# Performance work log

Hardware: AMD Instinct MI355X
Metric: run time of the kernel (lower is better)

## Reference

```python
import jax, jax.numpy as jnp
import numpy as np

B, L, D, H = 2, 2048, 2048, 16
Dh = D // H
THETA = 10000.0
NEG = -1e9


def _rope_tables(length, offset=0):
    # inv_freq: [Dh/2], positions: [L]
    inv_freq = 1.0 / (THETA ** (jnp.arange(0, Dh, 2, dtype=jnp.float32) / Dh))
    pos = jnp.arange(offset, offset + length, dtype=jnp.float32)
    freqs = pos[:, None] * inv_freq[None, :]           # [L, Dh/2]
    emb = jnp.concatenate([freqs, freqs], axis=-1)     # [L, Dh]
    return jnp.cos(emb), jnp.sin(emb)


def _rotate_half(t):
    t1, t2 = t[..., : Dh // 2], t[..., Dh // 2:]
    return jnp.concatenate([-t2, t1], axis=-1)


def setup_inputs() -> dict:
    key = jax.random.key(0)
    k1, k2, k3 = jax.random.split(key, 3)
    x = jax.random.normal(k1, (B, L, D), dtype=jnp.float32)
    attention_mask = jnp.ones((B, L), dtype=jnp.int32)
    w_qkv = jax.random.normal(k2, (D, 3 * D), dtype=jnp.float32) * (D ** -0.5)
    w_proj = jax.random.normal(k3, (D, D), dtype=jnp.float32) * (D ** -0.5)
    return {"x": x, "attention_mask": attention_mask, "w_qkv": w_qkv, "w_proj": w_proj}


def reference(x, attention_mask, w_qkv, w_proj):
    # QKV projection (no bias)
    qkv = x @ w_qkv                                    # [B, L, 3D]
    q, k, v = jnp.split(qkv, 3, axis=-1)
    q = q.reshape(B, L, H, Dh).transpose(0, 2, 1, 3)   # [B, H, L, Dh]
    k = k.reshape(B, L, H, Dh).transpose(0, 2, 1, 3)
    v = v.reshape(B, L, H, Dh).transpose(0, 2, 1, 3)

    # RoPE (past_len = 0)
    cos, sin = _rope_tables(L)                         # [L, Dh]
    q = q * cos + _rotate_half(q) * sin
    k = k * cos + _rotate_half(k) * sin

    # causal + key-padding mask (True = masked out)
    causal = jnp.triu(jnp.ones((L, L), dtype=bool), k=1)         # [L, L]
    pad = (attention_mask == 0)[:, None, None, :]                # [B,1,1,L]
    mask = causal[None, None, :, :] | pad                        # [B,1,L,L]

    scale = Dh ** -0.5
    scores = jnp.einsum("bhqd,bhkd->bhqk", q, k) * scale         # [B,H,L,L]
    scores = jnp.where(mask, NEG, scores)
    attn = jax.nn.softmax(scores, axis=-1)
    y = jnp.einsum("bhqk,bhkd->bhqd", attn, v)                   # [B,H,L,Dh]
    y = y.transpose(0, 2, 1, 3).reshape(B, L, D)
    return y @ w_proj
```

## Files before the change

kernel.cpp:

```cpp
#include <hip/hip_runtime.h>
#include <hip/hip_bf16.h>

typedef unsigned short ushort_t;
typedef __attribute__((ext_vector_type(4))) float fvec4;
typedef __attribute__((ext_vector_type(16))) float fvec16;
typedef __attribute__((ext_vector_type(8))) short short8;
typedef __attribute__((ext_vector_type(4))) unsigned short usvec4;
typedef __attribute__((ext_vector_type(2))) unsigned int uvec2;

typedef const __attribute__((address_space(1))) void* gas_ptr;
typedef __attribute__((address_space(3))) void* las_ptr;

__device__ __forceinline__ void glds16(const void* g, void* l) {
  __builtin_amdgcn_global_load_lds((gas_ptr)g, (las_ptr)l, 16, 0, 0);
}

__device__ __forceinline__ ushort_t f2bf(float f) {
  unsigned u = __float_as_uint(f);
  u += 0x7FFFu + ((u >> 16) & 1u);
  return (ushort_t)(u >> 16);
}
__device__ __forceinline__ float bf2f(ushort_t h) {
  return __uint_as_float(((unsigned)h) << 16);
}

__device__ __forceinline__ void swap32(unsigned& a, unsigned& b) {
#if __has_builtin(__builtin_amdgcn_permlane32_swap)
  uvec2 r = __builtin_amdgcn_permlane32_swap(a, b, false, false);
  a = r[0]; b = r[1];
#else
  const unsigned sa = (unsigned)__shfl_xor((int)a, 32);
  const unsigned sb = (unsigned)__shfl_xor((int)b, 32);
  const bool hi = (threadIdx.x & 32) != 0;
  const unsigned na = hi ? sb : a;
  const unsigned nb = hi ? b : sa;
  a = na; b = nb;
#endif
}

__global__ __launch_bounds__(256) void cast_f32_bf16(const float* __restrict__ X,
                                                     ushort_t* __restrict__ Xb) {
  const size_t i = ((size_t)blockIdx.x * 256 + threadIdx.x) * 4;
  const fvec4 v = *(const fvec4*)(X + i);
  usvec4 o;
  o[0] = f2bf(v[0]); o[1] = f2bf(v[1]); o[2] = f2bf(v[2]); o[3] = f2bf(v[3]);
  *(usvec4*)(Xb + i) = o;
}

__global__ __launch_bounds__(256) void tcast(const float* __restrict__ W,
                                             ushort_t* __restrict__ Wt,
                                             const int Kd, const int Nd) {
  __shared__ float ls[64][65];
  const int t = threadIdx.x;
  const int n0 = blockIdx.x * 64, k0 = blockIdx.y * 64;
  const int kr = t >> 4, nc = (t & 15) * 4;
#pragma unroll
  for (int it = 0; it < 4; ++it) {
    const fvec4 v = *(const fvec4*)(W + (size_t)(k0 + it * 16 + kr) * Nd + n0 + nc);
    ls[it * 16 + kr][nc + 0] = v[0];
    ls[it * 16 + kr][nc + 1] = v[1];
    ls[it * 16 + kr][nc + 2] = v[2];
    ls[it * 16 + kr][nc + 3] = v[3];
  }
  __syncthreads();
  const int nr = t >> 2, kg = (t & 3) * 16;
  __align__(16) ushort_t tmp[16];
#pragma unroll
  for (int i = 0; i < 16; ++i) tmp[i] = f2bf(ls[kg + i][nr]);
  ushort_t* dst = Wt + (size_t)(n0 + nr) * Kd + k0 + kg;
  *(short8*)(dst)     = *(const short8*)(tmp);
  *(short8*)(dst + 8) = *(const short8*)(tmp + 8);
}

__device__ __forceinline__ void stage_unit(const ushort_t* __restrict__ G, const int rbase,
                                           const int K, const int tk,
                                           ushort_t* ldsmat, const int u,
                                           const int wv, const int lane) {
  const int rr = lane >> 3;
  const int kk = ((lane & 7) ^ rr) * 8;
  const int r64 = wv * 8 + rr;
  glds16(G + (size_t)(rbase + u * 64 + r64) * K + tk + kk,
         ldsmat + (((u * 2 + 0) * 64 + wv * 8) * 64));
  glds16(G + (size_t)(rbase + 128 + u * 64 + r64) * K + tk + kk,
         ldsmat + (((u * 2 + 1) * 64 + wv * 8) * 64));
}

__device__ __forceinline__ short8 frag_ld(const ushort_t* ldsmat, const int rbase,
                                          const int kc, const int quad, const int mm) {
  const int r = rbase + mm;
  const int blk = r >> 6;
  const int pblk = ((blk & 1) << 1) | (blk >> 1);
  const int ldsrow = pblk * 64 + (r & 63);
  const int kb = (kc * 64 + quad * 16) ^ ((mm & 7) << 4);
  return *(const short8*)(ldsmat + ldsrow * 64 + (kb >> 1));
}

#define FENCE asm volatile("" ::: "memory")

#define LD_A4(s_, q_)                                                         \
  short8 af[2][2];                                                            \
  af[0][0] = frag_ld(&lds[s_][0][0], wr * 128 + (q_) * 32,      0, quad, mm); \
  af[0][1] = frag_ld(&lds[s_][0][0], wr * 128 + (q_) * 32,      1, quad, mm); \
  af[1][0] = frag_ld(&lds[s_][0][0], wr * 128 + (q_) * 32 + 16, 0, quad, mm); \
  af[1][1] = frag_ld(&lds[s_][0][0], wr * 128 + (q_) * 32 + 16, 1, quad, mm);

#define LD_B8(s_)                                                             \
  _Pragma("unroll")                                                           \
  for (int j = 0; j < 4; ++j) {                                               \
    bfr[j][0] = frag_ld(&lds[s_][1][0], wc * 64 + j * 16, 0, quad, mm);       \
    bfr[j][1] = frag_ld(&lds[s_][1][0], wc * 64 + j * 16, 1, quad, mm);       \
  }

#define MFMA16(q_)                                                            \
  __builtin_amdgcn_s_setprio(1);                                              \
  _Pragma("unroll")                                                           \
  for (int ii = 0; ii < 2; ++ii)                                              \
  _Pragma("unroll")                                                           \
  for (int j = 0; j < 4; ++j) {                                               \
    acc[(q_) * 2 + ii][j] = __builtin_amdgcn_mfma_f32_16x16x32_bf16(          \
        af[ii][0], bfr[j][0], acc[(q_) * 2 + ii][j], 0, 0, 0);                \
    acc[(q_) * 2 + ii][j] = __builtin_amdgcn_mfma_f32_16x16x32_bf16(          \
        af[ii][1], bfr[j][1], acc[(q_) * 2 + ii][j], 0, 0, 0);                \
  }                                                                           \
  __builtin_amdgcn_s_setprio(0);

__global__ __launch_bounds__(512, 2) void gemm256(
    const ushort_t* __restrict__ A, const ushort_t* __restrict__ Bt,
    const int M, const int N, const int K, const int mode,
    float* __restrict__ C,
    ushort_t* __restrict__ Qo, ushort_t* __restrict__ Ko, ushort_t* __restrict__ Vo) {
  __shared__ __align__(16) ushort_t lds[2][2][16384];

  const int tid = threadIdx.x, wv = tid >> 6, lane = tid & 63;
  const int quad = lane >> 4, mm = lane & 15;
  const int wr = wv >> 2, wc = wv & 3;

  const int nwg = gridDim.x, ntx = N >> 8;
  const int bid = blockIdx.x;
  const int swz = (bid & 7) * (nwg >> 3) + (bid >> 3);
  const int by = swz / ntx, bx = swz - by * ntx;
  const int row0 = by * 256, col0 = bx * 256;

  fvec4 acc[8][4];
#pragma unroll
  for (int i = 0; i < 8; ++i)
#pragma unroll
    for (int j = 0; j < 4; ++j) acc[i][j] = (fvec4){0.f, 0.f, 0.f, 0.f};

  short8 bfr[4][2];

  stage_unit(Bt, col0, K, 0,  &lds[0][1][0], 0, wv, lane); FENCE;
  stage_unit(Bt, col0, K, 0,  &lds[0][1][0], 1, wv, lane); FENCE;
  stage_unit(A,  row0, K, 0,  &lds[0][0][0], 0, wv, lane); FENCE;
  stage_unit(A,  row0, K, 0,  &lds[0][0][0], 1, wv, lane); FENCE;
  stage_unit(Bt, col0, K, 64, &lds[1][1][0], 0, wv, lane); FENCE;
  stage_unit(Bt, col0, K, 64, &lds[1][1][0], 1, wv, lane); FENCE;
  stage_unit(A,  row0, K, 64, &lds[1][0][0], 0, wv, lane); FENCE;
  asm volatile("s_waitcnt vmcnt(6)" ::: "memory");
  __builtin_amdgcn_s_barrier();

  const int nit = K >> 7;
  for (int i = 0; i < nit; ++i) {
    const bool more = (i + 1 < nit);
    const int kA = i * 128 + 64;
    const int kB = i * 128 + 128;
    const int kC = i * 128 + 192;
    {
      __builtin_amdgcn_s_barrier();
      LD_A4(0, 0);
      LD_B8(0);
      stage_unit(A, row0, K, kA, &lds[1][0][0], 1, wv, lane);
      MFMA16(0);
    }
    {
      __builtin_amdgcn_s_barrier();
      LD_A4(0, 1);
      if (more) stage_unit(Bt, col0, K, kB, &lds[0][1][0], 0, wv, lane);
      MFMA16(1);
    }
    {
      __builtin_amdgcn_s_barrier();
      LD_A4(0, 2);
      if (more) stage_unit(Bt, col0, K, kB, &lds[0][1][0], 1, wv, lane);
      MFMA16(2);
    }
    {
      __builtin_amdgcn_s_barrier();
      LD_A4(0, 3);
      if (more) {
        stage_unit(A, row0, K, kB, &lds[0][0][0], 0, wv, lane);
        asm volatile("s_waitcnt vmcnt(6)" ::: "memory");
      } else {
        asm volatile("s_waitcnt vmcnt(0)" ::: "memory");
      }
      MFMA16(3);
    }
    {
      __builtin_amdgcn_s_barrier();
      LD_A4(1, 0);
      LD_B8(1);
      if (more) stage_unit(A, row0, K, kB, &lds[0][0][0], 1, wv, lane);
      MFMA16(0);
    }
    {
      __builtin_amdgcn_s_barrier();
      LD_A4(1, 1);
      if (more) stage_unit(Bt, col0, K, kC, &lds[1][1][0], 0, wv, lane);
      MFMA16(1);
    }
    {
      __builtin_amdgcn_s_barrier();
      LD_A4(1, 2);
      if (more) stage_unit(Bt, col0, K, kC, &lds[1][1][0], 1, wv, lane);
      MFMA16(2);
    }
    {
      __builtin_amdgcn_s_barrier();
      LD_A4(1, 3);
      if (more) {
        stage_unit(A, row0, K, kC, &lds[1][0][0], 0, wv, lane);
        asm volatile("s_waitcnt vmcnt(6)" ::: "memory");
      }
      MFMA16(3);
    }
  }

  if (mode == 0) {
#pragma unroll
    for (int i = 0; i < 8; ++i)
#pragma unroll
      for (int r = 0; r < 4; ++r) {
        const int row = row0 + wr * 128 + i * 16 + quad * 4 + r;
        float* cr = C + (size_t)row * N + col0 + wc * 64;
#pragma unroll
        for (int j = 0; j < 4; ++j) cr[j * 16 + mm] = acc[i][j][r];
      }
  } else {
    const int gcol = col0 + wc * 64;
    const int which = gcol >> 11;
    const int h = (gcol >> 7) & 15;
    const int coff = gcol & 127;
    ushort_t* dst = (which == 0) ? Qo : (which == 1) ? Ko : Vo;
#pragma unroll
    for (int i = 0; i < 8; ++i)
#pragma unroll
      for (int r = 0; r < 4; ++r) {
        const int row = row0 + wr * 128 + i * 16 + quad * 4 + r;
        const int bb = row >> 11, l = row & 2047;
        ushort_t* dr = dst + ((size_t)(bb * 16 + h) * 2048 + l) * 128 + coff;
#pragma unroll
        for (int j = 0; j < 4; ++j) dr[j * 16 + mm] = f2bf(acc[i][j][r]);
      }
  }
}

__global__ __launch_bounds__(256) void rope_kernel(ushort_t* Qb, ushort_t* Kb) {
  const int gid = blockIdx.x * 256 + threadIdx.x;
  const int pd = gid & 63;
  const int row = gid >> 6;
  const int l = row & 2047;
  ushort_t* base = (blockIdx.y ? Kb : Qb) + (size_t)row * 128;
  const float a = bf2f(base[pd]);
  const float bv = bf2f(base[pd + 64]);
  const float invf_rev = exp2f(-(float)pd * 0.20762050593045702f) * 0.15915494309189535f;
  float rev = (float)l * invf_rev;
  rev -= floorf(rev);
  const float ang = rev * 6.283185307179586f;
  float s, c;
  __sincosf(ang, &s, &c);
  float na = a * c - bv * s;
  float nb = bv * c + a * s;
  if (blockIdx.y == 0) { na *= 0.08838834764831845f; nb *= 0.08838834764831845f; }
  base[pd] = f2bf(na);
  base[pd + 64] = f2bf(nb);
}

__global__ __launch_bounds__(256) void vtrans_kernel(const ushort_t* __restrict__ Vn,
                                                     ushort_t* __restrict__ Vt) {
  __shared__ ushort_t ls[128 * 132];
  const int bh = blockIdx.x >> 4;
  const int l0 = (blockIdx.x & 15) * 128;
  const int t = threadIdx.x;
  const ushort_t* src = Vn + ((size_t)bh * 2048 + l0) * 128;
#pragma unroll
  for (int it = 0; it < 16; ++it) {
    const int c = it * 256 + t;
    const int lr = c >> 5, dc = (c & 31) * 4;
    *(usvec4*)(ls + lr * 132 + dc) = *(const usvec4*)(src + lr * 128 + dc);
  }
  __syncthreads();
  ushort_t* dstb = Vt + (size_t)bh * 128 * 2048 + l0;
#pragma unroll
  for (int it = 0; it < 16; ++it) {
    const int c = it * 256 + t;
    const int d = c >> 5, lc = (c & 31) * 4;
    usvec4 o;
    o[0] = ls[(lc + 0) * 132 + d];
    o[1] = ls[(lc + 1) * 132 + d];
    o[2] = ls[(lc + 2) * 132 + d];
    o[3] = ls[(lc + 3) * 132 + d];
    *(usvec4*)(dstb + (size_t)d * 2048 + lc) = o;
  }
}

__global__ __launch_bounds__(256, 2) void flash_kernel(
    const ushort_t* __restrict__ Qb, const ushort_t* __restrict__ Kb,
    const ushort_t* __restrict__ Vt, const int* __restrict__ am,
    ushort_t* __restrict__ Y) {
  __shared__ __align__(16) ushort_t lK[2][8192];
  __shared__ __align__(16) ushort_t lV[2][8192];
  __shared__ float lds_l[128];

  const int tid = threadIdx.x, wv = tid >> 6, lane = tid & 63;
  const int lh = lane >> 5, cq = lane & 31;
  const int bid = blockIdx.x;
  const int bh = bid & 31;
  const int qi = 15 - (bid >> 5);
  const int b = bh >> 4, head = bh & 15;
  const size_t qkBase = (size_t)bh * (2048 * 128);
  const int qb = qi * 128 + wv * 32;
  const int q = qb + cq;

  short8 qf[8];
  {
    const ushort_t* qrow = Qb + qkBase + (size_t)q * 128;
#pragma unroll
    for (int c = 0; c < 8; ++c) qf[c] = *(const short8*)(qrow + c * 16 + lh * 8);
  }

  fvec16 yacc[4];
#pragma unroll
  for (int i = 0; i < 4; ++i)
#pragma unroll
    for (int r = 0; r < 16; ++r) yacc[i][r] = 0.f;
  float psum = 0.f;

#define FLASH_STAGE(dK, dV, kk0)                                                          \
  _Pragma("unroll")                                                                       \
  for (int it = 0; it < 4; ++it) {                                                        \
    const int f_ = it * 4 + wv;                                                           \
    const int ct_ = f_ >> 3, c_ = f_ & 7;                                                 \
    glds16(Kb + qkBase + (size_t)((kk0) + ct_ * 32 + cq) * 128 + c_ * 16 + lh * 8,        \
           (dK) + f_ * 512);                                                              \
    const int dt_ = f_ >> 2, kc_ = f_ & 3;                                                \
    glds16(Vt + ((size_t)bh * 128 + dt_ * 32 + cq) * 2048 + (kk0) + kc_ * 16 + lh * 8,    \
           (dV) + f_ * 512);                                                              \
  }

  const int nt = qi * 2 + 2;
  FLASH_STAGE(&lK[0][0], &lV[0][0], 0)
  __syncthreads();

  int cur = 0;
  for (int t = 0; t < nt; ++t) {
    const int k0 = t * 64;
    if (t + 1 < nt) {
      FLASH_STAGE(&lK[cur ^ 1][0], &lV[cur ^ 1][0], k0 + 64)
    }

    if (k0 <= qb + 31) {
      const ushort_t* bK = &lK[cur][0];
      const ushort_t* bV = &lV[cur][0];
      const int amv = am[b * 2048 + k0 + lane];
      const unsigned long long keymask = __ballot(amv != 0);
      const bool fullvalid = (k0 + 63 <= qb) && (keymask == ~0ull);

#pragma unroll
      for (int ct = 0; ct < 2; ++ct) {
        fvec16 sacc;
#pragma unroll
        for (int r = 0; r < 16; ++r) sacc[r] = 0.f;
        __builtin_amdgcn_s_setprio(1);
#pragma unroll
        for (int c = 0; c < 8; ++c) {
          short8 kf = *(const short8*)(bK + (ct * 8 + c) * 512 + lane * 8);
          sacc = __builtin_amdgcn_mfma_f32_32x32x16_bf16(kf, qf[c], sacc, 0, 0, 0);
        }
        __builtin_amdgcn_s_setprio(0);
        float p[16];
        if (fullvalid) {
#pragma unroll
          for (int r = 0; r < 16; ++r) p[r] = __expf(sacc[r]);
        } else {
#pragma unroll
          for (int r = 0; r < 16; ++r) {
            const int kl = (r & 3) + 8 * (r >> 2) + 4 * lh + ct * 32;
            const bool ok = (k0 + kl <= q) && (((keymask >> kl) & 1ull) != 0);
            p[r] = ok ? __expf(sacc[r]) : 0.f;
          }
        }
#pragma unroll
        for (int r = 0; r < 16; ++r) psum += p[r];
        unsigned pk[8];
#pragma unroll
        for (int j = 0; j < 8; ++j) {
          __hip_bfloat162 t2 = __float22bfloat162_rn(make_float2(p[2 * j], p[2 * j + 1]));
          pk[j] = *(unsigned*)&t2;
        }
#pragma unroll
        for (int kc2 = 0; kc2 < 2; ++kc2) {
          unsigned a0 = pk[kc2 * 4 + 0], a2 = pk[kc2 * 4 + 2];
          unsigned a1 = pk[kc2 * 4 + 1], a3 = pk[kc2 * 4 + 3];
          swap32(a0, a2);
          swap32(a1, a3);
          union { unsigned u[4]; short8 s; } pf;
          pf.u[0] = a0; pf.u[1] = a1; pf.u[2] = a2; pf.u[3] = a3;
          const int kc = ct * 2 + kc2;
          __builtin_amdgcn_s_setprio(1);
#pragma unroll
          for (int dt = 0; dt < 4; ++dt) {
            short8 vf = *(const short8*)(bV + (dt * 4 + kc) * 512 + lane * 8);
            yacc[dt] = __builtin_amdgcn_mfma_f32_32x32x16_bf16(pf.s, vf, yacc[dt], 0, 0, 0);
          }
          __builtin_amdgcn_s_setprio(0);
        }
      }
    }
    __syncthreads();
    cur ^= 1;
  }
#undef FLASH_STAGE

  psum += __shfl_xor(psum, 32);
  if (lane < 32) lds_l[wv * 32 + lane] = psum;
  float inv16[16];
#pragma unroll
  for (int r = 0; r < 16; ++r)
    inv16[r] = 1.f / lds_l[wv * 32 + (r & 3) + 8 * (r >> 2) + 4 * lh];

#pragma unroll
  for (int dt = 0; dt < 4; ++dt)
#pragma unroll
    for (int r = 0; r < 16; ++r) {
      const int qloc = (r & 3) + 8 * (r >> 2) + 4 * lh;
      ushort_t* dst = Y + ((size_t)(b * 2048 + qb + qloc)) * 2048 + head * 128 + dt * 32 + cq;
      *dst = f2bf(yacc[dt][r] * inv16[r]);
    }
}

extern "C" void kernel_launch(void* const* d_in, const int* in_sizes, int n_in,
                              void* d_out, int out_size, void* d_ws, size_t ws_size,
                              hipStream_t stream) {
  const float* x      = (const float*)d_in[0];
  const int*   amask  = (const int*)d_in[1];
  const float* w_qkv  = (const float*)d_in[2];
  const float* w_proj = (const float*)d_in[3];

  ushort_t* xb     = (ushort_t*)d_ws;
  ushort_t* wqkvT  = xb + 8388608;
  ushort_t* wprojT = wqkvT + 12582912;
  ushort_t* Qb     = wprojT + 4194304;
  ushort_t* Kb     = Qb + 8388608;
  ushort_t* Vn     = Kb + 8388608;
  ushort_t* Vt     = wqkvT;
  ushort_t* Yb     = xb;

  cast_f32_bf16<<<8192, 256, 0, stream>>>(x, xb);
  tcast<<<dim3(96, 32), 256, 0, stream>>>(w_qkv, wqkvT, 2048, 6144);
  tcast<<<dim3(32, 32), 256, 0, stream>>>(w_proj, wprojT, 2048, 2048);
  gemm256<<<384, 512, 0, stream>>>(xb, wqkvT, 4096, 6144, 2048, 1,
                                   nullptr, Qb, Kb, Vn);
  rope_kernel<<<dim3(16384, 2), 256, 0, stream>>>(Qb, Kb);
  vtrans_kernel<<<512, 256, 0, stream>>>(Vn, Vt);
  flash_kernel<<<512, 256, 0, stream>>>(Qb, Kb, Vt, amask, Yb);
  gemm256<<<128, 512, 0, stream>>>(Yb, wprojT, 4096, 2048, 2048, 0,
                                   (float*)d_out, nullptr, nullptr, nullptr);
}
```

Measured before the change: 399.0 us.

## Add 128x256 GEMM kernel, precompute mask bits, split score MFMA chains

Adds a new gemm128 kernel with 128x256 tiles and two blocks per CU, and uses it for both the QKV and output projections. This doubles the grid to improve occupancy and wave balance across CUs, at the cost of less reuse per tile. In the flash kernel, per-tile attention-mask validity is precomputed once into a bitmask so each tile no longer issues a global load and ballot. The QK^T MFMA chain is also split into two independent accumulators to cut dependency latency, which adds one extra add per score.

```diff
diff --git a/kernel.cpp b/kernel.cpp
--- a/kernel.cpp
+++ b/kernel.cpp
@@ -72,6 +72,8 @@
   *(short8*)(dst + 8) = *(const short8*)(tmp + 8);
 }
 
+#define FENCE asm volatile("" ::: "memory")
+
 __device__ __forceinline__ void stage_unit(const ushort_t* __restrict__ G, const int rbase,
                                            const int K, const int tk,
                                            ushort_t* ldsmat, const int u,
@@ -94,8 +96,6 @@
   const int kb = (kc * 64 + quad * 16) ^ ((mm & 7) << 4);
   return *(const short8*)(ldsmat + ldsrow * 64 + (kb >> 1));
 }
-
-#define FENCE asm volatile("" ::: "memory")
 
 #define LD_A4(s_, q_)                                                         \
   short8 af[2][2];                                                            \
@@ -165,64 +165,41 @@
     const int kA = i * 128 + 64;
     const int kB = i * 128 + 128;
     const int kC = i * 128 + 192;
-    {
-      __builtin_amdgcn_s_barrier();
-      LD_A4(0, 0);
-      LD_B8(0);
+    { __builtin_amdgcn_s_barrier();
+      LD_A4(0, 0); LD_B8(0);
       stage_unit(A, row0, K, kA, &lds[1][0][0], 1, wv, lane);
-      MFMA16(0);
-    }
-    {
-      __builtin_amdgcn_s_barrier();
+      MFMA16(0); }
+    { __builtin_amdgcn_s_barrier();
       LD_A4(0, 1);
       if (more) stage_unit(Bt, col0, K, kB, &lds[0][1][0], 0, wv, lane);
-      MFMA16(1);
-    }
-    {
-      __builtin_amdgcn_s_barrier();
+      MFMA16(1); }
+    { __builtin_amdgcn_s_barrier();
       LD_A4(0, 2);
       if (more) stage_unit(Bt, col0, K, kB, &lds[0][1][0], 1, wv, lane);
-      MFMA16(2);
-    }
-    {
-      __builtin_amdgcn_s_barrier();
+      MFMA16(2); }
+    { __builtin_amdgcn_s_barrier();
       LD_A4(0, 3);
-      if (more) {
-        stage_unit(A, row0, K, kB, &lds[0][0][0], 0, wv, lane);
+      if (more) { stage_unit(A, row0, K, kB, &lds[0][0][0], 0, wv, lane);
         asm volatile("s_waitcnt vmcnt(6)" ::: "memory");
-      } else {
-        asm volatile("s_waitcnt vmcnt(0)" ::: "memory");
-      }
-      MFMA16(3);
-    }
-    {
-      __builtin_amdgcn_s_barrier();
-      LD_A4(1, 0);
-      LD_B8(1);
+      } else { asm volatile("s_waitcnt vmcnt(0)" ::: "memory"); }
+      MFMA16(3); }
+    { __builtin_amdgcn_s_barrier();
+      LD_A4(1, 0); LD_B8(1);
       if (more) stage_unit(A, row0, K, kB, &lds[0][0][0], 1, wv, lane);
-      MFMA16(0);
-    }
-    {
-      __builtin_amdgcn_s_barrier();
+      MFMA16(0); }
+    { __builtin_amdgcn_s_barrier();
       LD_A4(1, 1);
       if (more) stage_unit(Bt, col0, K, kC, &lds[1][1][0], 0, wv, lane);
-      MFMA16(1);
-    }
-    {
-      __builtin_amdgcn_s_barrier();
+      MFMA16(1); }
+    { __builtin_amdgcn_s_barrier();
       LD_A4(1, 2);
       if (more) stage_unit(Bt, col0, K, kC, &lds[1][1][0], 1, wv, lane);
-      MFMA16(2);
-    }
-    {
-      __builtin_amdgcn_s_barrier();
+      MFMA16(2); }
+    { __builtin_amdgcn_s_barrier();
       LD_A4(1, 3);
-      if (more) {
-        stage_unit(A, row0, K, kC, &lds[1][0][0], 0, wv, lane);
-        asm volatile("s_waitcnt vmcnt(6)" ::: "memory");
-      }
-      MFMA16(3);
-    }
+      if (more) { stage_unit(A, row0, K, kC, &lds[1][0][0], 0, wv, lane);
+        asm volatile("s_waitcnt vmcnt(6)" ::: "memory"); }
+      MFMA16(3); }
   }
 
   if (mode == 0) {
@@ -250,6 +227,178 @@
         ushort_t* dr = dst + ((size_t)(bb * 16 + h) * 2048 + l) * 128 + coff;
 #pragma unroll
         for (int j = 0; j < 4; ++j) dr[j * 16 + mm] = f2bf(acc[i][j][r]);
+      }
+  }
+}
+
+__device__ __forceinline__ void stage_a128(const ushort_t* __restrict__ G, const int row0,
+                                           const int K, const int tk, ushort_t* ldsA,
+                                           const int wv, const int lane) {
+  const int rr = lane >> 3;
+  const int kk = ((lane & 7) ^ rr) * 8;
+  const int r = wv * 8 + rr;
+  glds16(G + (size_t)(row0 + r) * K + tk + kk,      ldsA + (wv * 8) * 64);
+  glds16(G + (size_t)(row0 + 64 + r) * K + tk + kk, ldsA + (64 + wv * 8) * 64);
+}
+__device__ __forceinline__ void stage_b128(const ushort_t* __restrict__ G, const int col0,
+                                           const int K, const int tk, ushort_t* ldsB,
+                                           const int u, const int wv, const int lane) {
+  const int rr = lane >> 3;
+  const int kk = ((lane & 7) ^ rr) * 8;
+  const int r = u * 64 + wv * 8 + rr;
+  glds16(G + (size_t)(col0 + r) * K + tk + kk,       ldsB + (u * 64 + wv * 8) * 64);
+  glds16(G + (size_t)(col0 + 128 + r) * K + tk + kk, ldsB + (128 + u * 64 + wv * 8) * 64);
+}
+__device__ __forceinline__ short8 fragld128(const ushort_t* mat, const int row,
+                                            const int kc, const int quad) {
+  const int kb = (kc * 64 + quad * 16) ^ ((row & 7) << 4);
+  return *(const short8*)(mat + row * 64 + (kb >> 1));
+}
+
+__global__ __launch_bounds__(512, 2) void gemm128(
+    const ushort_t* __restrict__ A, const ushort_t* __restrict__ Bt,
+    const int M, const int N, const int K, const int mode,
+    float* __restrict__ C,
+    ushort_t* __restrict__ Qo, ushort_t* __restrict__ Ko, ushort_t* __restrict__ Vo) {
+  __shared__ __align__(16) ushort_t l128[2][24576];
+
+  const int tid = threadIdx.x, wv = tid >> 6, lane = tid & 63;
+  const int quad = lane >> 4, mm = lane & 15;
+  const int wr = wv >> 2, wc = wv & 3;
+
+  const int nwg = gridDim.x, ntx = N >> 8;
+  const int bid = blockIdx.x;
+  const int swz = (bid & 7) * (nwg >> 3) + (bid >> 3);
+  const int by = swz / ntx, bx = swz - by * ntx;
+  const int row0 = by * 128, col0 = bx * 256;
+
+  fvec4 acc[4][4];
+#pragma unroll
+  for (int m = 0; m < 4; ++m)
+#pragma unroll
+    for (int j = 0; j < 4; ++j) acc[m][j] = (fvec4){0.f, 0.f, 0.f, 0.f};
+
+  ushort_t* A0 = &l128[0][0];     ushort_t* B0 = &l128[0][8192];
+  ushort_t* A1 = &l128[1][0];     ushort_t* B1 = &l128[1][8192];
+
+  short8 bfr[4][2];
+
+  stage_b128(Bt, col0, K, 0,  B0, 0, wv, lane); FENCE;
+  stage_b128(Bt, col0, K, 0,  B0, 1, wv, lane); FENCE;
+  stage_a128(A,  row0, K, 0,  A0,    wv, lane); FENCE;
+  stage_b128(Bt, col0, K, 64, B1, 0, wv, lane); FENCE;
+  stage_b128(Bt, col0, K, 64, B1, 1, wv, lane); FENCE;
+  asm volatile("s_waitcnt vmcnt(4)" ::: "memory");
+  __builtin_amdgcn_s_barrier();
+
+  const int nit = K >> 7;
+  for (int i = 0; i < nit; ++i) {
+    const bool more = (i + 1 < nit);
+    const int kA = i * 128 + 64;
+    const int kB = i * 128 + 128;
+    const int kC = i * 128 + 192;
+    {
+      stage_a128(A, row0, K, kA, A1, wv, lane);
+      short8 af[4];
+#pragma unroll
+      for (int m = 0; m < 4; ++m) af[m] = fragld128(A0, wr * 64 + m * 16 + mm, 0, quad);
+#pragma unroll
+      for (int j = 0; j < 4; ++j) {
+        bfr[j][0] = fragld128(B0, wc * 64 + j * 16 + mm, 0, quad);
+        bfr[j][1] = fragld128(B0, wc * 64 + j * 16 + mm, 1, quad);
+      }
+      __builtin_amdgcn_s_setprio(1);
+#pragma unroll
+      for (int m = 0; m < 4; ++m)
+#pragma unroll
+        for (int j = 0; j < 4; ++j)
+          acc[m][j] = __builtin_amdgcn_mfma_f32_16x16x32_bf16(af[m], bfr[j][0], acc[m][j], 0, 0, 0);
+      __builtin_amdgcn_s_setprio(0);
+      asm volatile("s_waitcnt lgkmcnt(0)" ::: "memory");
+      __builtin_amdgcn_sched_barrier(0);
+    }
+    {
+      __builtin_amdgcn_s_barrier();
+      if (more) { stage_b128(Bt, col0, K, kB, B0, 0, wv, lane); FENCE;
+                  stage_b128(Bt, col0, K, kB, B0, 1, wv, lane); FENCE; }
+      if (more) { asm volatile("s_waitcnt vmcnt(4)" ::: "memory"); }
+      else      { asm volatile("s_waitcnt vmcnt(0)" ::: "memory"); }
+      short8 af[4];
+#pragma unroll
+      for (int m = 0; m < 4; ++m) af[m] = fragld128(A0, wr * 64 + m * 16 + mm, 1, quad);
+      __builtin_amdgcn_s_setprio(1);
+#pragma unroll
+      for (int m = 0; m < 4; ++m)
+#pragma unroll
+        for (int j = 0; j < 4; ++j)
+          acc[m][j] = __builtin_amdgcn_mfma_f32_16x16x32_bf16(af[m], bfr[j][1], acc[m][j], 0, 0, 0);
+      __builtin_amdgcn_s_setprio(0);
+    }
+    {
+      __builtin_amdgcn_s_barrier();
+      if (more) stage_a128(A, row0, K, kB, A0, wv, lane);
+      short8 af[4];
+#pragma unroll
+      for (int m = 0; m < 4; ++m) af[m] = fragld128(A1, wr * 64 + m * 16 + mm, 0, quad);
+#pragma unroll
+      for (int j = 0; j < 4; ++j) {
+        bfr[j][0] = fragld128(B1, wc * 64 + j * 16 + mm, 0, quad);
+        bfr[j][1] = fragld128(B1, wc * 64 + j * 16 + mm, 1, quad);
+      }
+      __builtin_amdgcn_s_setprio(1);
+#pragma unroll
+      for (int m = 0; m < 4; ++m)
+#pragma unroll
+        for (int j = 0; j < 4; ++j)
+          acc[m][j] = __builtin_amdgcn_mfma_f32_16x16x32_bf16(af[m], bfr[j][0], acc[m][j], 0, 0, 0);
+      __builtin_amdgcn_s_setprio(0);
+      asm volatile("s_waitcnt lgkmcnt(0)" ::: "memory");
+      __builtin_amdgcn_sched_barrier(0);
+    }
+    {
+      __builtin_amdgcn_s_barrier();
+      if (more) { stage_b128(Bt, col0, K, kC, B1, 0, wv, lane); FENCE;
+                  stage_b128(Bt, col0, K, kC, B1, 1, wv, lane); FENCE;
+                  asm volatile("s_waitcnt vmcnt(4)" ::: "memory"); }
+      short8 af[4];
+#pragma unroll
+      for (int m = 0; m < 4; ++m) af[m] = fragld128(A1, wr * 64 + m * 16 + mm, 1, quad);
+      __builtin_amdgcn_s_setprio(1);
+#pragma unroll
+      for (int m = 0; m < 4; ++m)
+#pragma unroll
+        for (int j = 0; j < 4; ++j)
+          acc[m][j] = __builtin_amdgcn_mfma_f32_16x16x32_bf16(af[m], bfr[j][1], acc[m][j], 0, 0, 0);
+      __builtin_amdgcn_s_setprio(0);
+      __builtin_amdgcn_s_barrier();
+    }
+  }
+
+  if (mode == 0) {
+#pragma unroll
+    for (int m = 0; m < 4; ++m)
+#pragma unroll
+      for (int r = 0; r < 4; ++r) {
+        const int row = row0 + wr * 64 + m * 16 + quad * 4 + r;
+        float* cr = C + (size_t)row * N + col0 + wc * 64;
+#pragma unroll
+        for (int j = 0; j < 4; ++j) cr[j * 16 + mm] = acc[m][j][r];
+      }
+  } else {
+    const int gcol = col0 + wc * 64;
+    const int which = gcol >> 11;
+    const int h = (gcol >> 7) & 15;
+    const int coff = gcol & 127;
+    ushort_t* dst = (which == 0) ? Qo : (which == 1) ? Ko : Vo;
+#pragma unroll
+    for (int m = 0; m < 4; ++m)
+#pragma unroll
+      for (int r = 0; r < 4; ++r) {
+        const int row = row0 + wr * 64 + m * 16 + quad * 4 + r;
+        const int bb = row >> 11, l = row & 2047;
+        ushort_t* dr = dst + ((size_t)(bb * 16 + h) * 2048 + l) * 128 + coff;
+#pragma unroll
+        for (int j = 0; j < 4; ++j) dr[j * 16 + mm] = f2bf(acc[m][j][r]);
       }
   }
 }
@@ -321,6 +470,21 @@
   const int qb = qi * 128 + wv * 32;
   const int q = qb + cq;
 
+  unsigned fullbits = 0;
+  {
+    const int* amr = am + b * 2048;
+#pragma unroll
+    for (int rgn = 0; rgn < 4; ++rgn) {
+      const int4 a0 = *(const int4*)(amr + rgn * 512 + lane * 8);
+      const int4 a1 = *(const int4*)(amr + rgn * 512 + lane * 8 + 4);
+      const bool ok8 = a0.x && a0.y && a0.z && a0.w && a1.x && a1.y && a1.z && a1.w;
+      const unsigned long long bal = __ballot(ok8);
+#pragma unroll
+      for (int tt = 0; tt < 8; ++tt)
+        fullbits |= ((((bal >> (8 * tt)) & 0xFFull) == 0xFFull) ? 1u : 0u) << (rgn * 8 + tt);
+    }
+  }
+
   short8 qf[8];
   {
     const ushort_t* qrow = Qb + qkBase + (size_t)q * 128;
@@ -361,32 +525,38 @@
     if (k0 <= qb + 31) {
       const ushort_t* bK = &lK[cur][0];
       const ushort_t* bV = &lV[cur][0];
-      const int amv = am[b * 2048 + k0 + lane];
-      const unsigned long long keymask = __ballot(amv != 0);
-      const bool fullvalid = (k0 + 63 <= qb) && (keymask == ~0ull);
+      const bool maskfull = (fullbits >> t) & 1u;
+      unsigned long long keymask = ~0ull;
+      if (!maskfull) keymask = __ballot(am[b * 2048 + k0 + lane] != 0);
+      const bool fullvalid = (k0 + 63 <= qb) && maskfull;
 
 #pragma unroll
       for (int ct = 0; ct < 2; ++ct) {
-        fvec16 sacc;
-#pragma unroll
-        for (int r = 0; r < 16; ++r) sacc[r] = 0.f;
+        fvec16 sA_, sB_;
+#pragma unroll
+        for (int r = 0; r < 16; ++r) { sA_[r] = 0.f; sB_[r] = 0.f; }
         __builtin_amdgcn_s_setprio(1);
 #pragma unroll
-        for (int c = 0; c < 8; ++c) {
+        for (int c = 0; c < 4; ++c) {
           short8 kf = *(const short8*)(bK + (ct * 8 + c) * 512 + lane * 8);
-          sacc = __builtin_amdgcn_mfma_f32_32x32x16_bf16(kf, qf[c], sacc, 0, 0, 0);
+          sA_ = __builtin_amdgcn_mfma_f32_32x32x16_bf16(kf, qf[c], sA_, 0, 0, 0);
+        }
+#pragma unroll
+        for (int c = 4; c < 8; ++c) {
+          short8 kf = *(const short8*)(bK + (ct * 8 + c) * 512 + lane * 8);
+          sB_ = __builtin_amdgcn_mfma_f32_32x32x16_bf16(kf, qf[c], sB_, 0, 0, 0);
         }
         __builtin_amdgcn_s_setprio(0);
         float p[16];
         if (fullvalid) {
 #pragma unroll
-          for (int r = 0; r < 16; ++r) p[r] = __expf(sacc[r]);
+          for (int r = 0; r < 16; ++r) p[r] = __expf(sA_[r] + sB_[r]);
         } else {
 #pragma unroll
           for (int r = 0; r < 16; ++r) {
             const int kl = (r & 3) + 8 * (r >> 2) + 4 * lh + ct * 32;
             const bool ok = (k0 + kl <= q) && (((keymask >> kl) & 1ull) != 0);
-            p[r] = ok ? __expf(sacc[r]) : 0.f;
+            p[r] = ok ? __expf(sA_[r] + sB_[r]) : 0.f;
           }
         }
 #pragma unroll
@@ -458,11 +628,11 @@
   cast_f32_bf16<<<8192, 256, 0, stream>>>(x, xb);
   tcast<<<dim3(96, 32), 256, 0, stream>>>(w_qkv, wqkvT, 2048, 6144);
   tcast<<<dim3(32, 32), 256, 0, stream>>>(w_proj, wprojT, 2048, 2048);
-  gemm256<<<384, 512, 0, stream>>>(xb, wqkvT, 4096, 6144, 2048, 1,
+  gemm128<<<768, 512, 0, stream>>>(xb, wqkvT, 4096, 6144, 2048, 1,
                                    nullptr, Qb, Kb, Vn);
   rope_kernel<<<dim3(16384, 2), 256, 0, stream>>>(Qb, Kb);
   vtrans_kernel<<<512, 256, 0, stream>>>(Vn, Vt);
   flash_kernel<<<512, 256, 0, stream>>>(Qb, Kb, Vt, amask, Yb);
-  gemm256<<<128, 512, 0, stream>>>(Yb, wprojT, 4096, 2048, 2048, 0,
+  gemm128<<<256, 512, 0, stream>>>(Yb, wprojT, 4096, 2048, 2048, 0,
                                    (float*)d_out, nullptr, nullptr, nullptr);
 }
```

After: 390.7 us. 1.02x faster.
